# Kernel optimization log

Measured on AMD Instinct MI355X. Metric: run time of the kernel, lower is better.

## Reference

```python
import jax, jax.numpy as jnp
import numpy as np

B, Q, D, H, HD, P = 1, 2048, 2048, 16, 128, 512


def setup_inputs() -> dict:
    key = jax.random.key(0)
    ks = jax.random.split(key, 12)
    x = jax.random.normal(ks[0], (B, Q, D), jnp.float32)
    prefix_key = jax.random.normal(ks[1], (B, P, H, HD), jnp.float32)
    prefix_value = jax.random.normal(ks[2], (B, P, H, HD), jnp.float32)
    s = 1.0 / np.sqrt(D)
    Wq = jax.random.normal(ks[3], (D, H, HD), jnp.float32) * s
    Wk = jax.random.normal(ks[4], (D, H, HD), jnp.float32) * s
    Wv = jax.random.normal(ks[5], (D, H, HD), jnp.float32) * s
    bq = jnp.zeros((H, HD), jnp.float32)
    bk = jnp.zeros((H, HD), jnp.float32)
    bv = jnp.zeros((H, HD), jnp.float32)
    prefix_gate = jax.random.normal(ks[6], (H,), jnp.float32) * 0.1
    Wout = jax.random.normal(ks[7], (H, HD, D), jnp.float32) * (1.0 / np.sqrt(D))
    bout = jnp.zeros((D,), jnp.float32)
    # prefix fully visible, causal mask over the suffix (current sequence)
    causal = jnp.tril(jnp.ones((Q, Q), bool))
    mask = jnp.concatenate([jnp.ones((Q, P), bool), causal], axis=1)[None, None]  # [1,1,Q,P+Q]
    return dict(x=x, prefix_key=prefix_key, prefix_value=prefix_value,
                Wq=Wq, bq=bq, Wk=Wk, bk=bk, Wv=Wv, bv=bv,
                prefix_gate=prefix_gate, Wout=Wout, bout=bout, mask=mask)


def reference(x, prefix_key, prefix_value, Wq, bq, Wk, bk, Wv, bv, prefix_gate, Wout, bout, mask):
    head_dim = Wq.shape[-1]
    pl = prefix_key.shape[1]
    q = jnp.einsum('bqd,dhk->bqhk', x, Wq) + bq   # [B,Q,H,HD]
    k = jnp.einsum('bqd,dhk->bqhk', x, Wk) + bk
    v = jnp.einsum('bqd,dhk->bqhk', x, Wv) + bv
    k = jnp.concatenate([prefix_key, k], axis=1)   # [B,P+Q,H,HD]
    v = jnp.concatenate([prefix_value, v], axis=1)
    q = q / jnp.sqrt(jnp.asarray(head_dim, q.dtype))
    w = jnp.einsum('bqhd,bkhd->bhqk', q, k)        # [B,H,Q,P+Q]
    big_neg = jnp.finfo(w.dtype).min
    w = jnp.where(mask, w, big_neg)
    gate = prefix_gate[None, :, None, None]
    w_prefix = jax.nn.softmax(w[..., :pl]) * gate   # gated prefix segment
    w_suffix = jax.nn.softmax(w[..., pl:])          # regular suffix softmax
    w = jnp.concatenate([w_prefix, w_suffix], axis=-1)
    o = jnp.einsum('bhqk,bkhd->bqhd', w, v)         # [B,Q,H,HD]
    return jnp.einsum('bqhd,hdo->bqo', o, Wout) + bout
```

## Files before the change

kernel.cpp:

```cpp
#include <hip/hip_runtime.h>
#include <hip/hip_bf16.h>

typedef __bf16 bf16x8 __attribute__((ext_vector_type(8)));
typedef __bf16 bf16x4v __attribute__((ext_vector_type(4)));
typedef float f32x4 __attribute__((ext_vector_type(4)));

#define DMODEL 2048
#define NH 16
#define HD 128
#define PLEN 512
#define QLEN 2048
#define KVLEN 2560

__device__ __forceinline__ void gload_lds16(const void* g, void* l) {
  __builtin_amdgcn_global_load_lds((const __attribute__((address_space(1))) void*)g,
                                   (__attribute__((address_space(3))) void*)l, 16, 0, 0);
}


__global__ __launch_bounds__(256) void k_transpose_bf16(const float* __restrict__ in,
                                                        __bf16* __restrict__ out) {
  __shared__ float tile[64][65];
  const int t = threadIdx.x;
  const int tx = t & 63, ty = t >> 6;
  const int r0 = blockIdx.y * 64, c0 = blockIdx.x * 64;
#pragma unroll
  for (int i = 0; i < 16; ++i) {
    int r = ty + i * 4;
    tile[r][tx] = in[(size_t)(r0 + r) * DMODEL + c0 + tx];
  }
  __syncthreads();
#pragma unroll
  for (int i = 0; i < 16; ++i) {
    int r = ty + i * 4;
    out[(size_t)(c0 + r) * DMODEL + r0 + tx] = (__bf16)tile[tx][r];
  }
}

__global__ __launch_bounds__(256) void k_f32_to_bf16(const float* __restrict__ in,
                                                     __bf16* __restrict__ out, int n4) {
  int i = blockIdx.x * blockDim.x + threadIdx.x;
  int stride = gridDim.x * blockDim.x;
  for (; i < n4; i += stride) {
    float4 v = ((const float4*)in)[i];
    bf16x4v o;
    o[0] = (__bf16)v.x; o[1] = (__bf16)v.y; o[2] = (__bf16)v.z; o[3] = (__bf16)v.w;
    ((bf16x4v*)out)[i] = o;
  }
}

__global__ __launch_bounds__(256) void k_prefix(const float* __restrict__ pk,
                                                const float* __restrict__ pv,
                                                __bf16* __restrict__ Kall,
                                                __bf16* __restrict__ VT) {
  int idx = blockIdx.x * 256 + threadIdx.x;
  int hd = idx & 127;
  int h = (idx >> 7) & 15;
  int p = idx >> 11;
  Kall[(size_t)h * KVLEN * HD + (size_t)p * HD + hd] = (__bf16)pk[idx];
  VT[(size_t)h * HD * KVLEN + (size_t)hd * KVLEN + p] = (__bf16)pv[idx];
}


__device__ __forceinline__ void gemm_mainloop(const __bf16* __restrict__ A,
                                              const __bf16* __restrict__ BT,
                                              __bf16* Asm, __bf16* Bsm,
                                              int m0, int n0, int w, int l,
                                              f32x4 (&acc)[4][4]) {
  const int lr = l & 15, lg = l >> 4;
  const int lin0 = w * 2048 + l * 16;
  const int rowS = lin0 >> 6;
  const int colS = (lin0 & 63) >> 1;
  for (int k0 = 0; k0 < DMODEL; k0 += 32) {
    __syncthreads();
#pragma unroll
    for (int i = 0; i < 2; ++i) {
      const __bf16* ga = A + (size_t)(m0 + rowS + i * 16) * DMODEL + k0 + colS;
      gload_lds16(ga, (char*)Asm + w * 2048 + i * 1024);
      const __bf16* gb = BT + (size_t)(n0 + rowS + i * 16) * DMODEL + k0 + colS;
      gload_lds16(gb, (char*)Bsm + w * 2048 + i * 1024);
    }
    __syncthreads();
    bf16x8 af[4], bfv[4];
#pragma unroll
    for (int mi = 0; mi < 4; ++mi)
      af[mi] = *(const bf16x8*)(Asm + ((w >> 1) * 64 + mi * 16 + lr) * 32 + lg * 8);
#pragma unroll
    for (int ni = 0; ni < 4; ++ni)
      bfv[ni] = *(const bf16x8*)(Bsm + ((w & 1) * 64 + ni * 16 + lr) * 32 + lg * 8);
#pragma unroll
    for (int mi = 0; mi < 4; ++mi)
#pragma unroll
      for (int ni = 0; ni < 4; ++ni)
        acc[mi][ni] = __builtin_amdgcn_mfma_f32_16x16x32_bf16(af[mi], bfv[ni], acc[mi][ni], 0, 0, 0);
  }
}

__global__ __launch_bounds__(256) void gemm_qkv(const __bf16* __restrict__ xb,
                                                const __bf16* __restrict__ WqT,
                                                const __bf16* __restrict__ WkT,
                                                const __bf16* __restrict__ WvT,
                                                const float* __restrict__ bq,
                                                const float* __restrict__ bk,
                                                const float* __restrict__ bv,
                                                __bf16* __restrict__ Qs,
                                                __bf16* __restrict__ Kall,
                                                __bf16* __restrict__ VT) {
  __shared__ __bf16 Asm[4096];
  __shared__ __bf16 Bsm[4096];
  const int t = threadIdx.x, w = t >> 6, l = t & 63;
  const int m0 = blockIdx.x * 128, n0 = blockIdx.y * 128;
  const int z = blockIdx.z;
  const __bf16* BT = (z == 0) ? WqT : ((z == 1) ? WkT : WvT);
  const float* bias = (z == 0) ? bq : ((z == 1) ? bk : bv);
  f32x4 acc[4][4];
#pragma unroll
  for (int mi = 0; mi < 4; ++mi)
#pragma unroll
    for (int ni = 0; ni < 4; ++ni) acc[mi][ni] = (f32x4){0.f, 0.f, 0.f, 0.f};
  gemm_mainloop(xb, BT, Asm, Bsm, m0, n0, w, l, acc);
  const int lr = l & 15, lg = l >> 4;
#pragma unroll
  for (int mi = 0; mi < 4; ++mi)
#pragma unroll
    for (int ni = 0; ni < 4; ++ni)
#pragma unroll
      for (int r = 0; r < 4; ++r) {
        int row = m0 + (w >> 1) * 64 + mi * 16 + lg * 4 + r;
        int col = n0 + (w & 1) * 64 + ni * 16 + lr;
        float v = acc[mi][ni][r] + bias[col];
        int hh = col >> 7, hd = col & 127;
        if (z == 0) {
          Qs[(size_t)hh * QLEN * HD + (size_t)row * HD + hd] = (__bf16)(v * 0.08838834764831845f);
        } else if (z == 1) {
          Kall[(size_t)hh * KVLEN * HD + (size_t)(PLEN + row) * HD + hd] = (__bf16)v;
        } else {
          VT[(size_t)hh * HD * KVLEN + (size_t)hd * KVLEN + (PLEN + row)] = (__bf16)v;
        }
      }
}

__global__ __launch_bounds__(256) void gemm_out(const __bf16* __restrict__ Ob,
                                                const __bf16* __restrict__ WoT,
                                                const float* __restrict__ bout,
                                                float* __restrict__ out) {
  __shared__ __bf16 Asm[4096];
  __shared__ __bf16 Bsm[4096];
  const int t = threadIdx.x, w = t >> 6, l = t & 63;
  const int m0 = blockIdx.x * 128, n0 = blockIdx.y * 128;
  f32x4 acc[4][4];
#pragma unroll
  for (int mi = 0; mi < 4; ++mi)
#pragma unroll
    for (int ni = 0; ni < 4; ++ni) acc[mi][ni] = (f32x4){0.f, 0.f, 0.f, 0.f};
  gemm_mainloop(Ob, WoT, Asm, Bsm, m0, n0, w, l, acc);
  const int lr = l & 15, lg = l >> 4;
#pragma unroll
  for (int mi = 0; mi < 4; ++mi)
#pragma unroll
    for (int ni = 0; ni < 4; ++ni)
#pragma unroll
      for (int r = 0; r < 4; ++r) {
        int row = m0 + (w >> 1) * 64 + mi * 16 + lg * 4 + r;
        int col = n0 + (w & 1) * 64 + ni * 16 + lr;
        out[(size_t)row * DMODEL + col] = acc[mi][ni][r] + bout[col];
      }
}

template <int KS>
__global__ __launch_bounds__(256, 4) void k_attn(const __bf16* __restrict__ Qs,
                                                 const __bf16* __restrict__ Kall,
                                                 const __bf16* __restrict__ VT,
                                                 __bf16* __restrict__ P1buf,
                                                 float* __restrict__ S1buf,
                                                 __bf16* __restrict__ P2buf,
                                                 float* __restrict__ S2buf) {
  __shared__ __bf16 Ksm[2][4096];
  __shared__ __bf16 Vsm[2][4096];
  __shared__ __bf16 Pl[4][512];
  const int h = blockIdx.y, z = blockIdx.z, bx = blockIdx.x;
  const int t = threadIdx.x, w = t >> 6, l = t & 63;
  const int lr = l & 15, lg = l >> 4;
  const int q0 = bx * 64 + w * 16;
  const __bf16* Qh = Qs + (size_t)h * QLEN * HD;
  const char* Khb = (const char*)(Kall + (size_t)h * KVLEN * HD);
  const char* Vhb = (const char*)(VT + (size_t)h * HD * KVLEN);
  __bf16* Pw = &Pl[w][0];

  bf16x8 qf[4];
#pragma unroll
  for (int c = 0; c < 4; ++c)
    qf[c] = *(const bf16x8*)(Qh + (size_t)(q0 + lr) * HD + c * 32 + lg * 8);

  f32x4 acc[8];
  float ss[4];

  auto STAGE = [&](int buf, int kb) {
#pragma unroll
    for (int i = 0; i < 2; ++i) {
      int o = (i * 256 + w * 64 + l) * 16;
      int po = o ^ (((o >> 8) & 7) << 4);
      gload_lds16(Khb + (size_t)kb * 256 + po, (char*)&Ksm[buf][0] + i * 4096 + w * 1024);
    }
#pragma unroll
    for (int i = 0; i < 2; ++i) {
      int o = (i * 256 + w * 64 + l) * 16;
      int po = o ^ (((o >> 7) & 7) << 4);
      int row = po >> 6, colb = po & 63;
      gload_lds16(Vhb + (size_t)row * (KVLEN * 2) + (size_t)kb * 2 + colb,
                  (char*)&Vsm[buf][0] + i * 4096 + w * 1024);
    }
  };

  auto COMPUTE = [&](int buf, int mrel, bool domask) {
    const char* Kb = (const char*)&Ksm[buf][0];
    const char* Vb = (const char*)&Vsm[buf][0];
    f32x4 st0 = {0.f, 0.f, 0.f, 0.f}, st1 = {0.f, 0.f, 0.f, 0.f};
#pragma unroll
    for (int c = 0; c < 4; ++c) {
      int o0 = lr * 256 + c * 64 + lg * 16;        o0 ^= ((o0 >> 8) & 7) << 4;
      int o1 = (16 + lr) * 256 + c * 64 + lg * 16; o1 ^= ((o1 >> 8) & 7) << 4;
      bf16x8 kf0 = *(const bf16x8*)(Kb + o0);
      bf16x8 kf1 = *(const bf16x8*)(Kb + o1);
      st0 = __builtin_amdgcn_mfma_f32_16x16x32_bf16(qf[c], kf0, st0, 0, 0, 0);
      st1 = __builtin_amdgcn_mfma_f32_16x16x32_bf16(qf[c], kf1, st1, 0, 0, 0);
    }
#pragma unroll
    for (int r = 0; r < 4; ++r) {
      if (domask) {
        int qq = q0 + lg * 4 + r;
        if (mrel + lr > qq) st0[r] = -1e30f;
        if (mrel + 16 + lr > qq) st1[r] = -1e30f;
      }
      float p0 = __expf(st0[r] - 16.0f);
      float p1 = __expf(st1[r] - 16.0f);
      ss[r] += p0 + p1;
      Pw[(lg * 4 + r) * 32 + lr] = (__bf16)p0;
      Pw[(lg * 4 + r) * 32 + 16 + lr] = (__bf16)p1;
    }
    bf16x8 pf = *(const bf16x8*)(Pw + lr * 32 + lg * 8);
#pragma unroll
    for (int c = 0; c < 8; ++c) {
      int o = (c * 16 + lr) * 64 + lg * 16; o ^= ((o >> 7) & 7) << 4;
      bf16x8 vf = *(const bf16x8*)(Vb + o);
      acc[c] = __builtin_amdgcn_mfma_f32_16x16x32_bf16(pf, vf, acc[c], 0, 0, 0);
    }
  };

  auto STORE_PHASE = [&](__bf16* PBUF, float* SBUF) {
    const size_t rb = (size_t)(z * NH + h) * QLEN;
#pragma unroll
    for (int r = 0; r < 4; ++r) {
      float s = ss[r];
      s += __shfl_xor(s, 1); s += __shfl_xor(s, 2);
      s += __shfl_xor(s, 4); s += __shfl_xor(s, 8);
      const int row = q0 + lg * 4 + r;
      if (lr == 0) SBUF[rb + row] = s;
#pragma unroll
      for (int c = 0; c < 8; ++c)
        PBUF[(rb + row) * HD + c * 16 + lr] = (__bf16)acc[c][r];
    }
  };

#pragma unroll
  for (int c = 0; c < 8; ++c) acc[c] = (f32x4){0.f, 0.f, 0.f, 0.f};
#pragma unroll
  for (int r = 0; r < 4; ++r) ss[r] = 0.f;
  constexpr int NT1 = (PLEN / 32) / KS;
  int cur = 0;
  STAGE(0, z * 32);
  __syncthreads();
  for (int i = 0; i < NT1; ++i) {
    if (i + 1 < NT1) STAGE(cur ^ 1, (z + (i + 1) * KS) * 32);
    COMPUTE(cur, 0, false);
    __syncthreads();
    cur ^= 1;
  }
  STAGE(0, PLEN + z * 32);
  STORE_PHASE(P1buf, S1buf);

#pragma unroll
  for (int c = 0; c < 8; ++c) acc[c] = (f32x4){0.f, 0.f, 0.f, 0.f};
#pragma unroll
  for (int r = 0; r < 4; ++r) ss[r] = 0.f;
  const int ntb = 2 * bx + 2;
  const int n2 = (ntb - z + KS - 1) / KS;
  cur = 0;
  __syncthreads();
  for (int i = 0; i < n2; ++i) {
    const int tt = z + i * KS;
    if (i + 1 < n2) STAGE(cur ^ 1, PLEN + (z + (i + 1) * KS) * 32);
    COMPUTE(cur, tt * 32, tt * 32 + 31 > q0);
    __syncthreads();
    cur ^= 1;
  }
  STORE_PHASE(P2buf, S2buf);
}

template <int KS>
__global__ __launch_bounds__(256) void k_combine(const __bf16* __restrict__ P1buf,
                                                 const float* __restrict__ S1buf,
                                                 const __bf16* __restrict__ P2buf,
                                                 const float* __restrict__ S2buf,
                                                 const float* __restrict__ gate,
                                                 __bf16* __restrict__ Ob) {
  const int idx = blockIdx.x * 256 + threadIdx.x;
  const int d = idx & 127;
  const int q = (idx >> 7) & 2047;
  const int h = idx >> 18;
  const size_t rq = (size_t)h * QLEN + q;
  float a1 = 0.f, a2 = 0.f, s1 = 0.f, s2 = 0.f;
#pragma unroll
  for (int zz = 0; zz < KS; ++zz) {
    const size_t zb = (size_t)zz * NH * QLEN;
    a1 += (float)P1buf[(zb + rq) * HD + d];
    a2 += (float)P2buf[(zb + rq) * HD + d];
    s1 += S1buf[zb + rq];
    s2 += S2buf[zb + rq];
  }
  float o = a1 * (gate[h] / s1) + a2 / s2;
  Ob[(size_t)q * DMODEL + h * HD + d] = (__bf16)o;
}


extern "C" void kernel_launch(void* const* d_in, const int* in_sizes, int n_in,
                              void* d_out, int out_size, void* d_ws, size_t ws_size,
                              hipStream_t stream) {
  const float* x    = (const float*)d_in[0];
  const float* pk   = (const float*)d_in[1];
  const float* pv   = (const float*)d_in[2];
  const float* Wq   = (const float*)d_in[3];
  const float* bq   = (const float*)d_in[4];
  const float* Wk   = (const float*)d_in[5];
  const float* bk   = (const float*)d_in[6];
  const float* Wv   = (const float*)d_in[7];
  const float* bv   = (const float*)d_in[8];
  const float* gate = (const float*)d_in[9];
  const float* Wout = (const float*)d_in[10];
  const float* bout = (const float*)d_in[11];
  float* out = (float*)d_out;

  char* ws = (char*)d_ws;
  size_t off = 0;
  auto alc = [&](size_t bytes) -> char* {
    char* p = ws + off;
    off += bytes;
    off = (off + 255) & ~(size_t)255;
    return p;
  };
  __bf16* xb   = (__bf16*)alc((size_t)DMODEL * DMODEL * 2);
  __bf16* WqT  = (__bf16*)alc((size_t)DMODEL * DMODEL * 2);
  __bf16* WkT  = (__bf16*)alc((size_t)DMODEL * DMODEL * 2);
  __bf16* WvT  = (__bf16*)alc((size_t)DMODEL * DMODEL * 2);
  __bf16* WoT  = (__bf16*)alc((size_t)DMODEL * DMODEL * 2);
  __bf16* Qs   = (__bf16*)alc((size_t)NH * QLEN * HD * 2);
  __bf16* Kall = (__bf16*)alc((size_t)NH * KVLEN * HD * 2);
  __bf16* VTa  = (__bf16*)alc((size_t)NH * HD * KVLEN * 2);
  __bf16* Ob   = (__bf16*)alc((size_t)QLEN * DMODEL * 2);

  const size_t per_split = (size_t)NH * QLEN * HD * 2 * 2
                         + (size_t)NH * QLEN * 4 * 2 + 1024;
  int KS = (off + 2 * per_split <= ws_size) ? 2 : 1;
  __bf16* P1buf = (__bf16*)alc((size_t)KS * NH * QLEN * HD * 2);
  __bf16* P2buf = (__bf16*)alc((size_t)KS * NH * QLEN * HD * 2);
  float*  S1buf = (float*)alc((size_t)KS * NH * QLEN * 4);
  float*  S2buf = (float*)alc((size_t)KS * NH * QLEN * 4);

  dim3 tgrid(32, 32);
  k_transpose_bf16<<<tgrid, 256, 0, stream>>>(Wq, WqT);
  k_transpose_bf16<<<tgrid, 256, 0, stream>>>(Wk, WkT);
  k_transpose_bf16<<<tgrid, 256, 0, stream>>>(Wv, WvT);
  k_transpose_bf16<<<tgrid, 256, 0, stream>>>(Wout, WoT);
  k_f32_to_bf16<<<1024, 256, 0, stream>>>(x, xb, (DMODEL * DMODEL) / 4);
  k_prefix<<<4096, 256, 0, stream>>>(pk, pv, Kall, VTa);

  gemm_qkv<<<dim3(16, 16, 3), 256, 0, stream>>>(xb, WqT, WkT, WvT, bq, bk, bv, Qs, Kall, VTa);

  const int ncomb = (NH * QLEN * HD) / 256;
  if (KS == 2) {
    k_attn<2><<<dim3(32, 16, 2), 256, 0, stream>>>(Qs, Kall, VTa, P1buf, S1buf, P2buf, S2buf);
    k_combine<2><<<ncomb, 256, 0, stream>>>(P1buf, S1buf, P2buf, S2buf, gate, Ob);
  } else {
    k_attn<1><<<dim3(32, 16, 1), 256, 0, stream>>>(Qs, Kall, VTa, P1buf, S1buf, P2buf, S2buf);
    k_combine<1><<<ncomb, 256, 0, stream>>>(P1buf, S1buf, P2buf, S2buf, gate, Ob);
  }
  gemm_out<<<dim3(16, 16), 256, 0, stream>>>(Ob, WoT, bout, out);
}
```

Before: 227.1 us.

## Fuse attention combine, double-buffer GEMMs, narrow output tiles, balance causal tiles

Attention now keeps prefix and suffix accumulators in registers within one block and writes the gated, normalized output directly. This removes the K-split partial buffers and the separate combine kernel. Both GEMMs get a double-buffered LDS mainloop with MFMA priority hints, and the output GEMM uses 128x64 tiles to launch twice as many blocks. Attention also pads the P scratch rows against bank conflicts and reverses tile order for half the heads to balance causal work. The cost is less KV parallelism per query tile (no split), more registers and lower occupancy (launch bounds 2).

```diff
diff --git a/kernel.cpp b/kernel.cpp
--- a/kernel.cpp
+++ b/kernel.cpp
@@ -62,37 +62,69 @@
 }
 
 
-__device__ __forceinline__ void gemm_mainloop(const __bf16* __restrict__ A,
-                                              const __bf16* __restrict__ BT,
-                                              __bf16* Asm, __bf16* Bsm,
-                                              int m0, int n0, int w, int l,
-                                              f32x4 (&acc)[4][4]) {
+template <int BN>
+__device__ __forceinline__ void stage_tile(const __bf16* __restrict__ A,
+                                           const __bf16* __restrict__ BT,
+                                           char* AsmB, char* BsmB,
+                                           int m0, int n0, int k0, int w, int l) {
+#pragma unroll
+  for (int i = 0; i < 2; ++i) {
+    int base = i * 4096 + w * 1024;
+    int o = base + l * 16;
+    int row = o >> 6, col = (o & 63) >> 1;
+    gload_lds16(A + (size_t)(m0 + row) * DMODEL + k0 + col, AsmB + base);
+  }
+  if constexpr (BN == 128) {
+#pragma unroll
+    for (int i = 0; i < 2; ++i) {
+      int base = i * 4096 + w * 1024;
+      int o = base + l * 16;
+      int row = o >> 6, col = (o & 63) >> 1;
+      gload_lds16(BT + (size_t)(n0 + row) * DMODEL + k0 + col, BsmB + base);
+    }
+  } else {
+    int base = w * 1024;
+    int o = base + l * 16;
+    int row = o >> 6, col = (o & 63) >> 1;
+    gload_lds16(BT + (size_t)(n0 + row) * DMODEL + k0 + col, BsmB + base);
+  }
+}
+
+template <int BN>
+__device__ __forceinline__ void gemm_mainloop_db(const __bf16* __restrict__ A,
+                                                 const __bf16* __restrict__ BT,
+                                                 __bf16* Asm, __bf16* Bsm,
+                                                 int m0, int n0, int w, int l,
+                                                 f32x4 (&acc)[4][BN / 32]) {
+  constexpr int NI = BN / 32;
+  constexpr int ABUF = 4096;
+  constexpr int BBUF = BN * 32;
   const int lr = l & 15, lg = l >> 4;
-  const int lin0 = w * 2048 + l * 16;
-  const int rowS = lin0 >> 6;
-  const int colS = (lin0 & 63) >> 1;
+  int cur = 0;
+  stage_tile<BN>(A, BT, (char*)Asm, (char*)Bsm, m0, n0, 0, w, l);
+  __syncthreads();
   for (int k0 = 0; k0 < DMODEL; k0 += 32) {
+    if (k0 + 32 < DMODEL)
+      stage_tile<BN>(A, BT, (char*)(Asm + (cur ^ 1) * ABUF), (char*)(Bsm + (cur ^ 1) * BBUF),
+                     m0, n0, k0 + 32, w, l);
+    const __bf16* Ab = Asm + cur * ABUF;
+    const __bf16* Bb = Bsm + cur * BBUF;
+    bf16x8 af[4], bfv[NI];
+#pragma unroll
+    for (int mi = 0; mi < 4; ++mi)
+      af[mi] = *(const bf16x8*)(Ab + ((w >> 1) * 64 + mi * 16 + lr) * 32 + lg * 8);
+#pragma unroll
+    for (int ni = 0; ni < NI; ++ni)
+      bfv[ni] = *(const bf16x8*)(Bb + ((w & 1) * (BN / 2) + ni * 16 + lr) * 32 + lg * 8);
+    __builtin_amdgcn_s_setprio(1);
+#pragma unroll
+    for (int mi = 0; mi < 4; ++mi)
+#pragma unroll
+      for (int ni = 0; ni < NI; ++ni)
+        acc[mi][ni] = __builtin_amdgcn_mfma_f32_16x16x32_bf16(af[mi], bfv[ni], acc[mi][ni], 0, 0, 0);
+    __builtin_amdgcn_s_setprio(0);
     __syncthreads();
-#pragma unroll
-    for (int i = 0; i < 2; ++i) {
-      const __bf16* ga = A + (size_t)(m0 + rowS + i * 16) * DMODEL + k0 + colS;
-      gload_lds16(ga, (char*)Asm + w * 2048 + i * 1024);
-      const __bf16* gb = BT + (size_t)(n0 + rowS + i * 16) * DMODEL + k0 + colS;
-      gload_lds16(gb, (char*)Bsm + w * 2048 + i * 1024);
-    }
-    __syncthreads();
-    bf16x8 af[4], bfv[4];
-#pragma unroll
-    for (int mi = 0; mi < 4; ++mi)
-      af[mi] = *(const bf16x8*)(Asm + ((w >> 1) * 64 + mi * 16 + lr) * 32 + lg * 8);
-#pragma unroll
-    for (int ni = 0; ni < 4; ++ni)
-      bfv[ni] = *(const bf16x8*)(Bsm + ((w & 1) * 64 + ni * 16 + lr) * 32 + lg * 8);
-#pragma unroll
-    for (int mi = 0; mi < 4; ++mi)
-#pragma unroll
-      for (int ni = 0; ni < 4; ++ni)
-        acc[mi][ni] = __builtin_amdgcn_mfma_f32_16x16x32_bf16(af[mi], bfv[ni], acc[mi][ni], 0, 0, 0);
+    cur ^= 1;
   }
 }
 
@@ -106,8 +138,8 @@
                                                 __bf16* __restrict__ Qs,
                                                 __bf16* __restrict__ Kall,
                                                 __bf16* __restrict__ VT) {
-  __shared__ __bf16 Asm[4096];
-  __shared__ __bf16 Bsm[4096];
+  __shared__ __bf16 Asm[2][4096];
+  __shared__ __bf16 Bsm[2][4096];
   const int t = threadIdx.x, w = t >> 6, l = t & 63;
   const int m0 = blockIdx.x * 128, n0 = blockIdx.y * 128;
   const int z = blockIdx.z;
@@ -118,7 +150,7 @@
   for (int mi = 0; mi < 4; ++mi)
 #pragma unroll
     for (int ni = 0; ni < 4; ++ni) acc[mi][ni] = (f32x4){0.f, 0.f, 0.f, 0.f};
-  gemm_mainloop(xb, BT, Asm, Bsm, m0, n0, w, l, acc);
+  gemm_mainloop_db<128>(xb, BT, &Asm[0][0], &Bsm[0][0], m0, n0, w, l, acc);
   const int lr = l & 15, lg = l >> 4;
 #pragma unroll
   for (int mi = 0; mi < 4; ++mi)
@@ -144,44 +176,42 @@
                                                 const __bf16* __restrict__ WoT,
                                                 const float* __restrict__ bout,
                                                 float* __restrict__ out) {
-  __shared__ __bf16 Asm[4096];
-  __shared__ __bf16 Bsm[4096];
+  __shared__ __bf16 Asm[2][4096];
+  __shared__ __bf16 Bsm[2][2048];
   const int t = threadIdx.x, w = t >> 6, l = t & 63;
-  const int m0 = blockIdx.x * 128, n0 = blockIdx.y * 128;
-  f32x4 acc[4][4];
+  const int m0 = blockIdx.x * 128, n0 = blockIdx.y * 64;
+  f32x4 acc[4][2];
 #pragma unroll
   for (int mi = 0; mi < 4; ++mi)
 #pragma unroll
-    for (int ni = 0; ni < 4; ++ni) acc[mi][ni] = (f32x4){0.f, 0.f, 0.f, 0.f};
-  gemm_mainloop(Ob, WoT, Asm, Bsm, m0, n0, w, l, acc);
+    for (int ni = 0; ni < 2; ++ni) acc[mi][ni] = (f32x4){0.f, 0.f, 0.f, 0.f};
+  gemm_mainloop_db<64>(Ob, WoT, &Asm[0][0], &Bsm[0][0], m0, n0, w, l, acc);
   const int lr = l & 15, lg = l >> 4;
 #pragma unroll
   for (int mi = 0; mi < 4; ++mi)
 #pragma unroll
-    for (int ni = 0; ni < 4; ++ni)
+    for (int ni = 0; ni < 2; ++ni)
 #pragma unroll
       for (int r = 0; r < 4; ++r) {
         int row = m0 + (w >> 1) * 64 + mi * 16 + lg * 4 + r;
-        int col = n0 + (w & 1) * 64 + ni * 16 + lr;
+        int col = n0 + (w & 1) * 32 + ni * 16 + lr;
         out[(size_t)row * DMODEL + col] = acc[mi][ni][r] + bout[col];
       }
 }
 
-template <int KS>
-__global__ __launch_bounds__(256, 4) void k_attn(const __bf16* __restrict__ Qs,
+__global__ __launch_bounds__(256, 2) void k_attn(const __bf16* __restrict__ Qs,
                                                  const __bf16* __restrict__ Kall,
                                                  const __bf16* __restrict__ VT,
-                                                 __bf16* __restrict__ P1buf,
-                                                 float* __restrict__ S1buf,
-                                                 __bf16* __restrict__ P2buf,
-                                                 float* __restrict__ S2buf) {
+                                                 const float* __restrict__ gate,
+                                                 __bf16* __restrict__ Ob) {
   __shared__ __bf16 Ksm[2][4096];
   __shared__ __bf16 Vsm[2][4096];
-  __shared__ __bf16 Pl[4][512];
-  const int h = blockIdx.y, z = blockIdx.z, bx = blockIdx.x;
+  __shared__ __bf16 Pl[4][16 * 40];
+  const int h = blockIdx.y;
+  const int qt = (h < 8) ? blockIdx.x : (31 - blockIdx.x);
   const int t = threadIdx.x, w = t >> 6, l = t & 63;
   const int lr = l & 15, lg = l >> 4;
-  const int q0 = bx * 64 + w * 16;
+  const int q0 = qt * 64 + w * 16;
   const __bf16* Qh = Qs + (size_t)h * QLEN * HD;
   const char* Khb = (const char*)(Kall + (size_t)h * KVLEN * HD);
   const char* Vhb = (const char*)(VT + (size_t)h * HD * KVLEN);
@@ -192,8 +222,15 @@
   for (int c = 0; c < 4; ++c)
     qf[c] = *(const bf16x8*)(Qh + (size_t)(q0 + lr) * HD + c * 32 + lg * 8);
 
-  f32x4 acc[8];
-  float ss[4];
+  f32x4 acc1[8], acc2[8];
+  float ss1[4], ss2[4];
+#pragma unroll
+  for (int c = 0; c < 8; ++c) {
+    acc1[c] = (f32x4){0.f, 0.f, 0.f, 0.f};
+    acc2[c] = (f32x4){0.f, 0.f, 0.f, 0.f};
+  }
+#pragma unroll
+  for (int r = 0; r < 4; ++r) { ss1[r] = 0.f; ss2[r] = 0.f; }
 
   auto STAGE = [&](int buf, int kb) {
 #pragma unroll
@@ -212,10 +249,11 @@
     }
   };
 
-  auto COMPUTE = [&](int buf, int mrel, bool domask) {
+  auto COMPUTE = [&](int buf, int mrel, bool domask, f32x4 (&ACC)[8], float (&SS)[4]) {
     const char* Kb = (const char*)&Ksm[buf][0];
     const char* Vb = (const char*)&Vsm[buf][0];
     f32x4 st0 = {0.f, 0.f, 0.f, 0.f}, st1 = {0.f, 0.f, 0.f, 0.f};
+    __builtin_amdgcn_s_setprio(1);
 #pragma unroll
     for (int c = 0; c < 4; ++c) {
       int o0 = lr * 256 + c * 64 + lg * 16;        o0 ^= ((o0 >> 8) & 7) << 4;
@@ -225,6 +263,7 @@
       st0 = __builtin_amdgcn_mfma_f32_16x16x32_bf16(qf[c], kf0, st0, 0, 0, 0);
       st1 = __builtin_amdgcn_mfma_f32_16x16x32_bf16(qf[c], kf1, st1, 0, 0, 0);
     }
+    __builtin_amdgcn_s_setprio(0);
 #pragma unroll
     for (int r = 0; r < 4; ++r) {
       if (domask) {
@@ -234,92 +273,62 @@
       }
       float p0 = __expf(st0[r] - 16.0f);
       float p1 = __expf(st1[r] - 16.0f);
-      ss[r] += p0 + p1;
-      Pw[(lg * 4 + r) * 32 + lr] = (__bf16)p0;
-      Pw[(lg * 4 + r) * 32 + 16 + lr] = (__bf16)p1;
-    }
-    bf16x8 pf = *(const bf16x8*)(Pw + lr * 32 + lg * 8);
+      SS[r] += p0 + p1;
+      Pw[(lg * 4 + r) * 40 + lr] = (__bf16)p0;
+      Pw[(lg * 4 + r) * 40 + 16 + lr] = (__bf16)p1;
+    }
+    bf16x8 pf = *(const bf16x8*)(Pw + lr * 40 + lg * 8);
+    __builtin_amdgcn_s_setprio(1);
 #pragma unroll
     for (int c = 0; c < 8; ++c) {
       int o = (c * 16 + lr) * 64 + lg * 16; o ^= ((o >> 7) & 7) << 4;
       bf16x8 vf = *(const bf16x8*)(Vb + o);
-      acc[c] = __builtin_amdgcn_mfma_f32_16x16x32_bf16(pf, vf, acc[c], 0, 0, 0);
-    }
+      ACC[c] = __builtin_amdgcn_mfma_f32_16x16x32_bf16(pf, vf, ACC[c], 0, 0, 0);
+    }
+    __builtin_amdgcn_s_setprio(0);
   };
 
-  auto STORE_PHASE = [&](__bf16* PBUF, float* SBUF) {
-    const size_t rb = (size_t)(z * NH + h) * QLEN;
-#pragma unroll
-    for (int r = 0; r < 4; ++r) {
-      float s = ss[r];
-      s += __shfl_xor(s, 1); s += __shfl_xor(s, 2);
-      s += __shfl_xor(s, 4); s += __shfl_xor(s, 8);
-      const int row = q0 + lg * 4 + r;
-      if (lr == 0) SBUF[rb + row] = s;
-#pragma unroll
-      for (int c = 0; c < 8; ++c)
-        PBUF[(rb + row) * HD + c * 16 + lr] = (__bf16)acc[c][r];
-    }
-  };
-
-#pragma unroll
-  for (int c = 0; c < 8; ++c) acc[c] = (f32x4){0.f, 0.f, 0.f, 0.f};
-#pragma unroll
-  for (int r = 0; r < 4; ++r) ss[r] = 0.f;
-  constexpr int NT1 = (PLEN / 32) / KS;
   int cur = 0;
-  STAGE(0, z * 32);
+  STAGE(0, 0);
   __syncthreads();
-  for (int i = 0; i < NT1; ++i) {
-    if (i + 1 < NT1) STAGE(cur ^ 1, (z + (i + 1) * KS) * 32);
-    COMPUTE(cur, 0, false);
+#pragma unroll 1
+  for (int i = 0; i < PLEN / 32; ++i) {
+    if (i + 1 < PLEN / 32) STAGE(cur ^ 1, (i + 1) * 32);
+    COMPUTE(cur, 0, false, acc1, ss1);
     __syncthreads();
     cur ^= 1;
   }
-  STAGE(0, PLEN + z * 32);
-  STORE_PHASE(P1buf, S1buf);
-
-#pragma unroll
-  for (int c = 0; c < 8; ++c) acc[c] = (f32x4){0.f, 0.f, 0.f, 0.f};
-#pragma unroll
-  for (int r = 0; r < 4; ++r) ss[r] = 0.f;
-  const int ntb = 2 * bx + 2;
-  const int n2 = (ntb - z + KS - 1) / KS;
+
+  const int ntb = 2 * qt + 2;
   cur = 0;
+  STAGE(0, PLEN);
   __syncthreads();
-  for (int i = 0; i < n2; ++i) {
-    const int tt = z + i * KS;
-    if (i + 1 < n2) STAGE(cur ^ 1, PLEN + (z + (i + 1) * KS) * 32);
-    COMPUTE(cur, tt * 32, tt * 32 + 31 > q0);
+#pragma unroll 1
+  for (int i = 0; i < ntb; ++i) {
+    if (i + 1 < ntb) STAGE(cur ^ 1, PLEN + (i + 1) * 32);
+    COMPUTE(cur, i * 32, i * 32 + 31 > q0, acc2, ss2);
     __syncthreads();
     cur ^= 1;
   }
-  STORE_PHASE(P2buf, S2buf);
-}
-
-template <int KS>
-__global__ __launch_bounds__(256) void k_combine(const __bf16* __restrict__ P1buf,
-                                                 const float* __restrict__ S1buf,
-                                                 const __bf16* __restrict__ P2buf,
-                                                 const float* __restrict__ S2buf,
-                                                 const float* __restrict__ gate,
-                                                 __bf16* __restrict__ Ob) {
-  const int idx = blockIdx.x * 256 + threadIdx.x;
-  const int d = idx & 127;
-  const int q = (idx >> 7) & 2047;
-  const int h = idx >> 18;
-  const size_t rq = (size_t)h * QLEN + q;
-  float a1 = 0.f, a2 = 0.f, s1 = 0.f, s2 = 0.f;
-#pragma unroll
-  for (int zz = 0; zz < KS; ++zz) {
-    const size_t zb = (size_t)zz * NH * QLEN;
-    a1 += (float)P1buf[(zb + rq) * HD + d];
-    a2 += (float)P2buf[(zb + rq) * HD + d];
-    s1 += S1buf[zb + rq];
-    s2 += S2buf[zb + rq];
-  }
-  float o = a1 * (gate[h] / s1) + a2 / s2;
-  Ob[(size_t)q * DMODEL + h * HD + d] = (__bf16)o;
+
+  const float g = gate[h];
+#pragma unroll
+  for (int r = 0; r < 4; ++r) {
+    float s1 = ss1[r];
+    s1 += __shfl_xor(s1, 1); s1 += __shfl_xor(s1, 2);
+    s1 += __shfl_xor(s1, 4); s1 += __shfl_xor(s1, 8);
+    float s2 = ss2[r];
+    s2 += __shfl_xor(s2, 1); s2 += __shfl_xor(s2, 2);
+    s2 += __shfl_xor(s2, 4); s2 += __shfl_xor(s2, 8);
+    const float f1 = g / s1;
+    const float f2 = 1.0f / s2;
+    const int qrow = q0 + lg * 4 + r;
+#pragma unroll
+    for (int c = 0; c < 8; ++c) {
+      float val = acc1[c][r] * f1 + acc2[c][r] * f2;
+      Ob[(size_t)qrow * DMODEL + h * HD + c * 16 + lr] = (__bf16)val;
+    }
+  }
 }
 
 
@@ -358,14 +367,6 @@
   __bf16* VTa  = (__bf16*)alc((size_t)NH * HD * KVLEN * 2);
   __bf16* Ob   = (__bf16*)alc((size_t)QLEN * DMODEL * 2);
 
-  const size_t per_split = (size_t)NH * QLEN * HD * 2 * 2
-                         + (size_t)NH * QLEN * 4 * 2 + 1024;
-  int KS = (off + 2 * per_split <= ws_size) ? 2 : 1;
-  __bf16* P1buf = (__bf16*)alc((size_t)KS * NH * QLEN * HD * 2);
-  __bf16* P2buf = (__bf16*)alc((size_t)KS * NH * QLEN * HD * 2);
-  float*  S1buf = (float*)alc((size_t)KS * NH * QLEN * 4);
-  float*  S2buf = (float*)alc((size_t)KS * NH * QLEN * 4);
-
   dim3 tgrid(32, 32);
   k_transpose_bf16<<<tgrid, 256, 0, stream>>>(Wq, WqT);
   k_transpose_bf16<<<tgrid, 256, 0, stream>>>(Wk, WkT);
@@ -375,14 +376,6 @@
   k_prefix<<<4096, 256, 0, stream>>>(pk, pv, Kall, VTa);
 
   gemm_qkv<<<dim3(16, 16, 3), 256, 0, stream>>>(xb, WqT, WkT, WvT, bq, bk, bv, Qs, Kall, VTa);
-
-  const int ncomb = (NH * QLEN * HD) / 256;
-  if (KS == 2) {
-    k_attn<2><<<dim3(32, 16, 2), 256, 0, stream>>>(Qs, Kall, VTa, P1buf, S1buf, P2buf, S2buf);
-    k_combine<2><<<ncomb, 256, 0, stream>>>(P1buf, S1buf, P2buf, S2buf, gate, Ob);
-  } else {
-    k_attn<1><<<dim3(32, 16, 1), 256, 0, stream>>>(Qs, Kall, VTa, P1buf, S1buf, P2buf, S2buf);
-    k_combine<1><<<ncomb, 256, 0, stream>>>(P1buf, S1buf, P2buf, S2buf, gate, Ob);
-  }
-  gemm_out<<<dim3(16, 16), 256, 0, stream>>>(Ob, WoT, bout, out);
-}
+  k_attn<<<dim3(32, 16), 256, 0, stream>>>(Qs, Kall, VTa, gate, Ob);
+  gemm_out<<<dim3(16, 32), 256, 0, stream>>>(Ob, WoT, bout, out);
+}
```

Result: faster. 221.1 us (-2.6%).
